# Kernel tuning notes

Measured on AMD Instinct MI355X. Metric: run time of the kernel, lower is better.

The kernel has to match this reference:

```python
import jax, jax.numpy as jnp
import numpy as np

B, N, E = 4, 25000, 1600000
NODE_DIM, EMBED = 64, 64
NUM = B * N


def setup_inputs() -> dict:
    key = jax.random.key(0)
    ks = jax.random.split(key, 12)
    p = lambda k, s: jax.random.normal(k, s, jnp.float32) * 0.05
    z = lambda s: jnp.zeros(s, jnp.float32)
    return {
        "node_feat": jax.random.normal(ks[0], (B, N, NODE_DIM), jnp.float32),
        "src": jax.random.randint(ks[1], (E,), 0, NUM),
        "dst": jax.random.randint(ks[2], (E,), 0, NUM),
        "edge_weight": jax.random.uniform(ks[3], (E,), jnp.float32),
        "h": z((NUM, EMBED)),
        "W_cz": p(ks[4], (NODE_DIM, EMBED)), "b_cz": z((EMBED,)),
        "W_cr": p(ks[5], (NODE_DIM, EMBED)), "b_cr": z((EMBED,)),
        "W_ch": p(ks[6], (NODE_DIM, EMBED)), "b_ch": z((EMBED,)),
        "W_lz": p(ks[7], (2 * EMBED, EMBED)), "b_lz": z((EMBED,)),
        "W_lr": p(ks[8], (2 * EMBED, EMBED)), "b_lr": z((EMBED,)),
        "W_lh": p(ks[9], (2 * EMBED, EMBED)), "b_lh": z((EMBED,)),
        "W_head": p(ks[10], (EMBED, 1)), "b_head": z((1,)),
    }


def gcn_conv(x, W, b, src, dst, ew):
    # PyG GCNConv: self-loops (fill=1) + symmetric normalization, then linear.
    n = x.shape[0]
    loop = jnp.arange(n)
    s = jnp.concatenate([src, loop])
    d = jnp.concatenate([dst, loop])
    w = jnp.concatenate([ew, jnp.ones((n,), x.dtype)])
    deg = jax.ops.segment_sum(w, d, num_segments=n)
    dinv = jnp.where(deg > 0, jax.lax.rsqrt(deg), 0.0)
    norm = dinv[s] * w * dinv[d]                      # [E+n]
    xw = x @ W                                        # [n, EMBED]
    out = jax.ops.segment_sum(xw[s] * norm[:, None], d, num_segments=n)
    return out + b


def tgcn_cell(x, h, src, dst, ew,
              W_cz, b_cz, W_cr, b_cr, W_ch, b_ch,
              W_lz, b_lz, W_lr, b_lr, W_lh, b_lh):
    Z = jax.nn.sigmoid(
        jnp.concatenate([gcn_conv(x, W_cz, b_cz, src, dst, ew), h], axis=1) @ W_lz + b_lz)
    R = jax.nn.sigmoid(
        jnp.concatenate([gcn_conv(x, W_cr, b_cr, src, dst, ew), h], axis=1) @ W_lr + b_lr)
    H_tilde = jnp.tanh(
        jnp.concatenate([gcn_conv(x, W_ch, b_ch, src, dst, ew), h * R], axis=1) @ W_lh + b_lh)
    return Z * h + (1.0 - Z) * H_tilde


def reference(node_feat, src, dst, edge_weight, h,
              W_cz, b_cz, W_cr, b_cr, W_ch, b_ch,
              W_lz, b_lz, W_lr, b_lr, W_lh, b_lh,
              W_head, b_head):
    Bv, Nv, _ = node_feat.shape
    x = node_feat.reshape(Bv * Nv, -1)
    h0 = tgcn_cell(x, h, src, dst, edge_weight,
                   W_cz, b_cz, W_cr, b_cr, W_ch, b_ch,
                   W_lz, b_lz, W_lr, b_lr, W_lh, b_lh)
    z = jax.nn.relu(h0)
    z = (z @ W_head + b_head).reshape(Bv, Nv, -1)
    return (z, h0)
```

## Files before the change

### kernel.cpp

```cpp
#include <hip/hip_runtime.h>
#include <hip/hip_fp16.h>
#include <stdint.h>

typedef unsigned long long u64;
typedef _Float16 half8 __attribute__((ext_vector_type(8)));
typedef float f32x4 __attribute__((ext_vector_type(4)));

#define EPB 6144
#define CAPC 5440

__device__ __forceinline__ float sigm(float x) { return 1.0f / (1.0f + __expf(-x)); }
__device__ __forceinline__ float tanhfast(float x) { return 1.0f - 2.0f / (__expf(2.0f * x) + 1.0f); }
__device__ __forceinline__ int rli(int v, int k) { return __builtin_amdgcn_readlane(v, k); }
__device__ __forceinline__ float rlf(float v, int k) {
    return __int_as_float(__builtin_amdgcn_readlane(__float_as_int(v), k));
}

__global__ void k_pre(const float* __restrict__ Wcz, const float* __restrict__ bcz,
                      const float* __restrict__ Wcr, const float* __restrict__ bcr,
                      const float* __restrict__ Wch, const float* __restrict__ bch,
                      const float* __restrict__ Wlz, const float* __restrict__ blz,
                      const float* __restrict__ Wlr, const float* __restrict__ blr,
                      const float* __restrict__ Wlh, const float* __restrict__ blh,
                      const float4* __restrict__ h4, __half* __restrict__ aggh,
                      __half* __restrict__ B1f, __half* __restrict__ B2f,
                      float* __restrict__ bias, int* __restrict__ cursor, int hq) {
    int bid = blockIdx.x;
    if (bid < 113) {
        int tid = bid * 256 + threadIdx.x;
        if (tid < 1024) cursor[tid] = 0;
        if (tid < 24576) {
            int k = tid / 192, nc = tid % 192;
            int g = nc >> 6, j = nc & 63;
            const float* Wc = (g == 0) ? Wcz : (g == 1) ? Wcr : Wch;
            const float* Wl = (g == 0) ? Wlz : (g == 1) ? Wlr : Wlh;
            float v;
            if (k < 64) {
                float acc = 0.f;
                for (int m = 0; m < 64; m++) acc += Wc[k * 64 + m] * Wl[m * 64 + j];
                v = acc;
            } else {
                v = (g < 2) ? Wl[k * 64 + j] : 0.f;
            }
            int kt = k >> 5, nt = nc >> 4;
            int lane = (((k >> 3) & 3) << 4) | (nc & 15);
            B1f[(((kt * 12 + nt) * 64 + lane) << 3) + (k & 7)] = (__half)v;
        } else if (tid < 24576 + 4096) {
            int t = tid - 24576;
            int k = t >> 6, nc = t & 63;
            float v = Wlh[(64 + k) * 64 + nc];
            int kt = k >> 5, nt = nc >> 4;
            int lane = (((k >> 3) & 3) << 4) | (nc & 15);
            B2f[(((kt * 4 + nt) * 64 + lane) << 3) + (k & 7)] = (__half)v;
        } else if (tid < 24576 + 4096 + 192) {
            int t = tid - 24576 - 4096;
            int g = t >> 6, j = t & 63;
            const float* bc = (g == 0) ? bcz : (g == 1) ? bcr : bch;
            const float* Wl = (g == 0) ? Wlz : (g == 1) ? Wlr : Wlh;
            const float* bl = (g == 0) ? blz : (g == 1) ? blr : blh;
            float acc = bl[j];
            for (int m = 0; m < 64; m++) acc += bc[m] * Wl[m * 64 + j];
            bias[t] = acc;
        }
    } else {
        int i = (bid - 113) * 256 + threadIdx.x;
        if (i < hq) {
            float4 hv = h4[i];
            int elem = i * 4;
            int node = elem >> 6, c = elem & 63;
            __half2* ho = (__half2*)(aggh + (((size_t)node) << 7) + 64 + c);
            ho[0] = __floats2half2_rn(hv.x, hv.y);
            ho[1] = __floats2half2_rn(hv.z, hv.w);
        }
    }
}

__global__ void __launch_bounds__(1024) k_bin(const int* __restrict__ src, const int* __restrict__ dst,
                                              const float* __restrict__ ew,
                                              int* __restrict__ cursor, u64* __restrict__ binned,
                                              int E, int R) {
    __shared__ u64 recs[EPB];
    __shared__ int hist[512];
    __shared__ int loff[512];
    __shared__ int curL[512];
    __shared__ int gbase[512];

    int tid = threadIdx.x;
    if (tid < 512) hist[tid] = 0;
    __syncthreads();

    int base = blockIdx.x * EPB;
    int cntE = min(EPB, E - base);

    u64 myrec[6];
    int myr[6];
#pragma unroll
    for (int j = 0; j < 6; j++) {
        int idx = tid + j * 1024;
        if (idx < cntE) {
            int e = base + idx;
            int d = dst[e], s = src[e];
            float w = ew[e];
            int r = d >> 8;
            myr[j] = r;
            myrec[j] = (u64)((unsigned)s | ((unsigned)(d & 255) << 17)) | ((u64)__float_as_uint(w) << 32);
            atomicAdd(&hist[r], 1);
        } else myr[j] = -1;
    }
    __syncthreads();

    if (tid < 64) {
        int sums[8], tot = 0;
#pragma unroll
        for (int q = 0; q < 8; q++) { sums[q] = hist[tid * 8 + q]; tot += sums[q]; }
        int scan = tot;
#pragma unroll
        for (int o = 1; o < 64; o <<= 1) {
            int v = __shfl_up(scan, o);
            if (tid >= o) scan += v;
        }
        int run = scan - tot;
#pragma unroll
        for (int q = 0; q < 8; q++) { loff[tid * 8 + q] = run; run += sums[q]; }
    }
    if (tid < 512) curL[tid] = 0;
    if (tid < R) {
        int hcnt = hist[tid];
        if (hcnt > 0) gbase[tid] = tid * CAPC + atomicAdd(&cursor[tid], hcnt);
    }
    __syncthreads();

#pragma unroll
    for (int j = 0; j < 6; j++) {
        if (myr[j] >= 0) {
            int p = atomicAdd(&curL[myr[j]], 1);
            recs[loff[myr[j]] + p] = myrec[j];
        }
    }
    __syncthreads();

    int wave = tid >> 6, lane = tid & 63;
    for (int r = wave; r < R; r += 16) {
        int len = hist[r];
        if (!len) continue;
        int gb = gbase[r], lo = loff[r];
        int capEnd = (r + 1) * CAPC;
        for (int i = lane; i < len; i += 64)
            if (gb + i < capEnd) binned[(size_t)(gb + i)] = recs[lo + i];
    }
}

__global__ void __launch_bounds__(1024) k_sort(const int* __restrict__ cursor,
                                               u64* __restrict__ binned,
                                               const float2* __restrict__ x2,
                                               float* __restrict__ dinv,
                                               __half2* __restrict__ xs2,
                                               int* __restrict__ off_g, int* __restrict__ len_g,
                                               int n) {
    __shared__ u64 srt[CAPC];
    __shared__ int hist[256];
    __shared__ int noff[256];
    __shared__ int cur[256];
    __shared__ u64 degw64[256];
    __shared__ float dvS[256];

    int r = blockIdx.x, tid = threadIdx.x;
    if (tid < 256) { hist[tid] = 0; degw64[tid] = 0ULL; }
    __syncthreads();

    int cnt = min(cursor[r], CAPC);
    u64* B = binned + (size_t)r * CAPC;

    for (int i = tid; i < cnt; i += 1024) {
        u64 m = B[i];
        int dl = ((unsigned)m >> 17) & 255;
        atomicAdd(&hist[dl], 1);
        float w = __uint_as_float((unsigned)(m >> 32));
        atomicAdd(&degw64[dl], (u64)(w * 4294967296.0f));
    }
    __syncthreads();

    if (tid < 64) {
        int s0 = hist[tid * 4], s1 = hist[tid * 4 + 1], s2 = hist[tid * 4 + 2], s3 = hist[tid * 4 + 3];
        int tot = s0 + s1 + s2 + s3;
        int scan = tot;
#pragma unroll
        for (int o = 1; o < 64; o <<= 1) {
            int v = __shfl_up(scan, o);
            if (tid >= o) scan += v;
        }
        int run = scan - tot;
        noff[tid * 4] = run; run += s0;
        noff[tid * 4 + 1] = run; run += s1;
        noff[tid * 4 + 2] = run; run += s2;
        noff[tid * 4 + 3] = run;
    }
    __syncthreads();

    if (tid < 256) {
        int node = r * 256 + tid;
        float deg = (float)degw64[tid] * 0x1p-32f;
        float dv = rsqrtf(1.0f + deg);
        if (node < n) {
            dinv[node] = dv;
            off_g[node] = r * CAPC + noff[tid];
            len_g[node] = hist[tid];
        }
        cur[tid] = noff[tid];
        dvS[tid] = dv;
    }
    __syncthreads();

    for (int i = tid; i < cnt; i += 1024) {
        u64 m = B[i];
        int dl = ((unsigned)m >> 17) & 255;
        int p = atomicAdd(&cur[dl], 1);
        srt[p] = (u64)((unsigned)m & 0x1FFFF) | (m & 0xFFFFFFFF00000000ULL);
    }
    __syncthreads();

    for (int i = tid; i < cnt; i += 1024) B[i] = srt[i];
    int nbase = r * 256;
    for (int i = tid; i < 256 * 32; i += 1024) {
        int nl = i >> 5, cp = i & 31;
        int node = nbase + nl;
        if (node < n) {
            float2 xv = x2[((size_t)node << 5) + cp];
            float dv = dvS[nl];
            xs2[((size_t)node << 5) + cp] = __floats2half2_rn(dv * xv.x, dv * xv.y);
        }
    }
}

__global__ void __launch_bounds__(256) k_gather(const int* __restrict__ off_g, const int* __restrict__ len_g,
                                                const u64* __restrict__ csr, const float* __restrict__ dinv,
                                                const __half* __restrict__ xs,
                                                __half* __restrict__ aggh, int n) {
    int lane = threadIdx.x & 63;
    int wid = __builtin_amdgcn_readfirstlane(threadIdx.x >> 6);
    int d = blockIdx.x * 4 + wid;
    if (d >= n) return;
    int o0 = off_g[d], L = len_g[d];
    float dd = dinv[d];
    float acc[16];
#pragma unroll
    for (int j = 0; j < 16; j++) acc[j] = 0.f;
    acc[0] = (float)xs[((size_t)d << 6) + lane];

    for (int base = 0; base < L; base += 64) {
        int c = min(64, L - base);
        u64 m = (lane < c) ? csr[(size_t)(o0 + base) + lane] : 0;
        int s_l = (unsigned)m & 0x1FFFF;
        float w_l = __uint_as_float((unsigned)(m >> 32));
        int k = 0;
        for (; k + 16 <= c; k += 16) {
            int ss[16]; float ww[16], xr[16];
#pragma unroll
            for (int j = 0; j < 16; j++) { ss[j] = rli(s_l, k + j); ww[j] = rlf(w_l, k + j); }
#pragma unroll
            for (int j = 0; j < 16; j++) xr[j] = (float)xs[((size_t)ss[j] << 6) + lane];
#pragma unroll
            for (int j = 0; j < 16; j++) acc[j] = fmaf(ww[j], xr[j], acc[j]);
        }
        for (; k + 4 <= c; k += 4) {
            int ss[4]; float ww[4], xr[4];
#pragma unroll
            for (int j = 0; j < 4; j++) { ss[j] = rli(s_l, k + j); ww[j] = rlf(w_l, k + j); }
#pragma unroll
            for (int j = 0; j < 4; j++) xr[j] = (float)xs[((size_t)ss[j] << 6) + lane];
#pragma unroll
            for (int j = 0; j < 4; j++) acc[j] = fmaf(ww[j], xr[j], acc[j]);
        }
        for (; k < c; k++) {
            int s0 = rli(s_l, k);
            float w0 = rlf(w_l, k);
            acc[0] = fmaf(w0, (float)xs[((size_t)s0 << 6) + lane], acc[0]);
        }
    }
    float s = ((acc[0] + acc[1]) + (acc[2] + acc[3])) + ((acc[4] + acc[5]) + (acc[6] + acc[7]))
            + ((acc[8] + acc[9]) + (acc[10] + acc[11])) + ((acc[12] + acc[13]) + (acc[14] + acc[15]));
    aggh[((size_t)d << 7) + lane] = (__half)(dd * s);
}

__global__ void __launch_bounds__(256, 2) k_node(
        const __half* __restrict__ aggh,
        const __half* __restrict__ B1f_g, const __half* __restrict__ B2f_g,
        const float* __restrict__ bias_g, const float* __restrict__ Whead,
        const float* __restrict__ bhead,
        float* __restrict__ out_head, float* __restrict__ out_h, int n) {

    __shared__ __half B1s[24576];
    __shared__ __half B2s[4096];
    __shared__ float biasS[192];
    __shared__ float whS[64];
    __shared__ __half hrb[4][16 * 72];

    int tid = threadIdx.x;
    {
        const uint4* s1 = (const uint4*)B1f_g; uint4* d1 = (uint4*)B1s;
        for (int i = tid; i < 3072; i += 256) d1[i] = s1[i];
        const uint4* s2 = (const uint4*)B2f_g; uint4* d2 = (uint4*)B2s;
        for (int i = tid; i < 512; i += 256) d2[i] = s2[i];
        if (tid < 192) biasS[tid] = bias_g[tid];
        if (tid < 64) whS[tid] = Whead[tid];
    }
    __syncthreads();

    int lane = tid & 63;
    int wave = tid >> 6;
    int quad = lane >> 4;
    int l15 = lane & 15;

    float bz4[4], br4[4], bh4[4], wh4[4];
#pragma unroll
    for (int nt = 0; nt < 4; nt++) {
        bz4[nt] = biasS[nt * 16 + l15];
        br4[nt] = biasS[64 + nt * 16 + l15];
        bh4[nt] = biasS[128 + nt * 16 + l15];
        wh4[nt] = whS[nt * 16 + l15];
    }
    float bhv = bhead[0];
    __half* myhr = &hrb[wave][0];
    const half8* B1v = (const half8*)B1s;
    const half8* B2v = (const half8*)B2s;

    int mbase = blockIdx.x * 64 + wave * 16;
    if (mbase < n) {
        const half8* arow = (const half8*)(aggh + (((size_t)(mbase + l15)) << 7) + (quad << 3));
        half8 a0 = arow[0], a1 = arow[4], a2 = arow[8], a3 = arow[12];

        f32x4 acc[12];
#pragma unroll
        for (int nt = 0; nt < 12; nt++) acc[nt] = (f32x4){0.f, 0.f, 0.f, 0.f};

#pragma unroll
        for (int nt = 0; nt < 12; nt++) {
            acc[nt] = __builtin_amdgcn_mfma_f32_16x16x32_f16(a0, B1v[(0 * 12 + nt) * 64 + lane], acc[nt], 0, 0, 0);
            acc[nt] = __builtin_amdgcn_mfma_f32_16x16x32_f16(a1, B1v[(1 * 12 + nt) * 64 + lane], acc[nt], 0, 0, 0);
            acc[nt] = __builtin_amdgcn_mfma_f32_16x16x32_f16(a2, B1v[(2 * 12 + nt) * 64 + lane], acc[nt], 0, 0, 0);
            acc[nt] = __builtin_amdgcn_mfma_f32_16x16x32_f16(a3, B1v[(3 * 12 + nt) * 64 + lane], acc[nt], 0, 0, 0);
        }

        float hv[4][4];
#pragma unroll
        for (int nt = 0; nt < 4; nt++)
#pragma unroll
            for (int r = 0; r < 4; r++)
                hv[nt][r] = (float)aggh[(((size_t)(mbase + quad * 4 + r)) << 7) + 64 + nt * 16 + l15];

        float Z[4][4];
#pragma unroll
        for (int nt = 0; nt < 4; nt++)
#pragma unroll
            for (int r = 0; r < 4; r++) {
                Z[nt][r] = sigm(acc[nt][r] + bz4[nt]);
                float R = sigm(acc[4 + nt][r] + br4[nt]);
                myhr[(quad * 4 + r) * 72 + nt * 16 + l15] = (__half)(hv[nt][r] * R);
            }
        __builtin_amdgcn_s_waitcnt(0);

        half8 a2f0 = *(const half8*)(myhr + l15 * 72 + quad * 8);
        half8 a2f1 = *(const half8*)(myhr + l15 * 72 + 32 + quad * 8);

#pragma unroll
        for (int nt = 0; nt < 4; nt++) {
            acc[8 + nt] = __builtin_amdgcn_mfma_f32_16x16x32_f16(a2f0, B2v[(0 * 4 + nt) * 64 + lane], acc[8 + nt], 0, 0, 0);
            acc[8 + nt] = __builtin_amdgcn_mfma_f32_16x16x32_f16(a2f1, B2v[(1 * 4 + nt) * 64 + lane], acc[8 + nt], 0, 0, 0);
        }

        float pr0 = 0.f, pr1 = 0.f, pr2 = 0.f, pr3 = 0.f;
#pragma unroll
        for (int nt = 0; nt < 4; nt++) {
#pragma unroll
            for (int r = 0; r < 4; r++) {
                float Ht = tanhfast(acc[8 + nt][r] + bh4[nt]);
                float z = Z[nt][r];
                float hn = z * hv[nt][r] + (1.f - z) * Ht;
                out_h[((size_t)(mbase + quad * 4 + r)) * 64 + nt * 16 + l15] = hn;
                float rv = fmaxf(hn, 0.f) * wh4[nt];
                if (r == 0) pr0 += rv; else if (r == 1) pr1 += rv; else if (r == 2) pr2 += rv; else pr3 += rv;
            }
        }
#pragma unroll
        for (int o = 1; o < 16; o <<= 1) {
            pr0 += __shfl_xor(pr0, o);
            pr1 += __shfl_xor(pr1, o);
            pr2 += __shfl_xor(pr2, o);
            pr3 += __shfl_xor(pr3, o);
        }
        if (l15 == 0) {
            out_head[mbase + quad * 4 + 0] = pr0 + bhv;
            out_head[mbase + quad * 4 + 1] = pr1 + bhv;
            out_head[mbase + quad * 4 + 2] = pr2 + bhv;
            out_head[mbase + quad * 4 + 3] = pr3 + bhv;
        }
    }
}

extern "C" void kernel_launch(void* const* d_in, const int* in_sizes, int n_in,
                              void* d_out, int out_size, void* d_ws, size_t ws_size,
                              hipStream_t stream) {
    const float* x     = (const float*)d_in[0];
    const int*   src   = (const int*)d_in[1];
    const int*   dst   = (const int*)d_in[2];
    const float* ew    = (const float*)d_in[3];
    const float* h     = (const float*)d_in[4];
    const float* Wcz   = (const float*)d_in[5];
    const float* bcz   = (const float*)d_in[6];
    const float* Wcr   = (const float*)d_in[7];
    const float* bcr   = (const float*)d_in[8];
    const float* Wch   = (const float*)d_in[9];
    const float* bch   = (const float*)d_in[10];
    const float* Wlz   = (const float*)d_in[11];
    const float* blz   = (const float*)d_in[12];
    const float* Wlr   = (const float*)d_in[13];
    const float* blr   = (const float*)d_in[14];
    const float* Wlh   = (const float*)d_in[15];
    const float* blh   = (const float*)d_in[16];
    const float* Whead = (const float*)d_in[17];
    const float* bhead = (const float*)d_in[18];

    int E = in_sizes[1];
    int n = in_sizes[4] / 64;
    int R = (n + 255) >> 8;

    __half* aggh = (__half*)d_ws;
    __half* xs   = aggh + (size_t)n * 128;
    u64*   binned = (u64*)(xs + (size_t)n * 64);
    float* dinv  = (float*)(binned + (size_t)R * CAPC);
    int*   off_g = (int*)(dinv + n);
    int*   len_g = off_g + n;
    int*   cursor = len_g + n;
    __half* B1f  = (__half*)(cursor + 1024);
    __half* B2f  = B1f + 24576;
    float* bias  = (float*)(B2f + 4096);

    float* out_head = (float*)d_out;
    float* out_h    = out_head + n;

    int hq = n * 16;
    int nbB = (E + EPB - 1) / EPB;
    int gridPre = 113 + (hq + 255) / 256;

    k_pre<<<gridPre, 256, 0, stream>>>(Wcz, bcz, Wcr, bcr, Wch, bch,
                                       Wlz, blz, Wlr, blr, Wlh, blh,
                                       (const float4*)h, aggh, B1f, B2f, bias, cursor, hq);
    k_bin<<<nbB, 1024, 0, stream>>>(src, dst, ew, cursor, binned, E, R);
    k_sort<<<R, 1024, 0, stream>>>(cursor, binned, (const float2*)x, dinv,
                                   (__half2*)xs, off_g, len_g, n);
    k_gather<<<(n + 3) / 4, 256, 0, stream>>>(off_g, len_g, binned, dinv, xs, aggh, n);
    k_node<<<(n + 63) / 64, 256, 0, stream>>>(aggh, B1f, B2f, bias, Whead, bhead,
                                              out_head, out_h, n);
}
```

Measured before the change: 235.2 us.

## Build CSR with global atomic counting, block scan and atomic scatter

Replaces the two-level LDS binning and per-bin sort with a direct CSR build. A per-edge global 64-bit atomic packs the in-degree count and the fixed-point weighted degree for each destination node. A block-level scan then turns counts into offsets, taking each block's base from an atomic cursor, and a final pass scatters each edge into its slot with a per-node atomic cursor. This removes the staging buffer with fixed per-bin capacity and its extra read/write passes, but adds many contended global atomics and random 8-byte writes. Edge order within a node, and the placement of node ranges, become nondeterministic.

Result: slower. 413.9 us (+76.0%).

```diff
diff --git a/kernel.cpp b/kernel.cpp
--- a/kernel.cpp
+++ b/kernel.cpp
@@ -5,9 +5,6 @@
 typedef unsigned long long u64;
 typedef _Float16 half8 __attribute__((ext_vector_type(8)));
 typedef float f32x4 __attribute__((ext_vector_type(4)));
-
-#define EPB 6144
-#define CAPC 5440
 
 __device__ __forceinline__ float sigm(float x) { return 1.0f / (1.0f + __expf(-x)); }
 __device__ __forceinline__ float tanhfast(float x) { return 1.0f - 2.0f / (__expf(2.0f * x) + 1.0f); }
@@ -16,19 +13,26 @@
     return __int_as_float(__builtin_amdgcn_readlane(__float_as_int(v), k));
 }
 
-__global__ void k_pre(const float* __restrict__ Wcz, const float* __restrict__ bcz,
-                      const float* __restrict__ Wcr, const float* __restrict__ bcr,
-                      const float* __restrict__ Wch, const float* __restrict__ bch,
-                      const float* __restrict__ Wlz, const float* __restrict__ blz,
-                      const float* __restrict__ Wlr, const float* __restrict__ blr,
-                      const float* __restrict__ Wlh, const float* __restrict__ blh,
-                      const float4* __restrict__ h4, __half* __restrict__ aggh,
-                      __half* __restrict__ B1f, __half* __restrict__ B2f,
-                      float* __restrict__ bias, int* __restrict__ cursor, int hq) {
+__global__ void k_zero(u64* __restrict__ cntdeg, int* __restrict__ gcur, int n) {
+    int i = blockIdx.x * 256 + threadIdx.x;
+    if (i < n) cntdeg[i] = 0ULL;
+    if (i < 16) gcur[i] = 0;
+}
+
+__global__ void k_prec(const float* __restrict__ Wcz, const float* __restrict__ bcz,
+                       const float* __restrict__ Wcr, const float* __restrict__ bcr,
+                       const float* __restrict__ Wch, const float* __restrict__ bch,
+                       const float* __restrict__ Wlz, const float* __restrict__ blz,
+                       const float* __restrict__ Wlr, const float* __restrict__ blr,
+                       const float* __restrict__ Wlh, const float* __restrict__ blh,
+                       const float4* __restrict__ h4, __half* __restrict__ aggh,
+                       __half* __restrict__ B1f, __half* __restrict__ B2f,
+                       float* __restrict__ bias,
+                       const int* __restrict__ dst, const float* __restrict__ ew,
+                       u64* __restrict__ cntdeg, int hq, int E, int hb) {
     int bid = blockIdx.x;
     if (bid < 113) {
         int tid = bid * 256 + threadIdx.x;
-        if (tid < 1024) cursor[tid] = 0;
         if (tid < 24576) {
             int k = tid / 192, nc = tid % 192;
             int g = nc >> 6, j = nc & 63;
@@ -62,7 +66,7 @@
             for (int m = 0; m < 64; m++) acc += bc[m] * Wl[m * 64 + j];
             bias[t] = acc;
         }
-    } else {
+    } else if (bid < 113 + hb) {
         int i = (bid - 113) * 256 + threadIdx.x;
         if (i < hq) {
             float4 hv = h4[i];
@@ -72,164 +76,88 @@
             ho[0] = __floats2half2_rn(hv.x, hv.y);
             ho[1] = __floats2half2_rn(hv.z, hv.w);
         }
-    }
-}
-
-__global__ void __launch_bounds__(1024) k_bin(const int* __restrict__ src, const int* __restrict__ dst,
-                                              const float* __restrict__ ew,
-                                              int* __restrict__ cursor, u64* __restrict__ binned,
-                                              int E, int R) {
-    __shared__ u64 recs[EPB];
-    __shared__ int hist[512];
-    __shared__ int loff[512];
-    __shared__ int curL[512];
-    __shared__ int gbase[512];
+    } else {
+        int e = (bid - 113 - hb) * 256 + threadIdx.x;
+        if (e < E) {
+            int d = dst[e];
+            float w = ew[e];
+            atomicAdd(&cntdeg[d], (1ULL << 48) | (u64)(w * 4294967296.0f));
+        }
+    }
+}
+
+__global__ void __launch_bounds__(1024) k_scan(const u64* __restrict__ cntdeg,
+                                               const float2* __restrict__ x2,
+                                               int* __restrict__ off_g, int* __restrict__ len_g,
+                                               int* __restrict__ cur_g, float* __restrict__ dinv,
+                                               __half2* __restrict__ xs2,
+                                               int* __restrict__ gcur, int n) {
+    __shared__ int wsum[16];
+    __shared__ int sbase;
+    __shared__ float dvS[1024];
 
     int tid = threadIdx.x;
-    if (tid < 512) hist[tid] = 0;
+    int nb = blockIdx.x * 1024;
+    int node = nb + tid;
+    u64 v = (node < n) ? cntdeg[node] : 0ULL;
+    int c = (int)(v >> 48);
+    float deg = (float)(v & 0xFFFFFFFFFFFFULL) * 0x1p-32f;
+
+    int lane = tid & 63, wv = tid >> 6;
+    int scan = c;
+#pragma unroll
+    for (int o = 1; o < 64; o <<= 1) {
+        int t = __shfl_up(scan, o);
+        if (lane >= o) scan += t;
+    }
+    if (lane == 63) wsum[wv] = scan;
     __syncthreads();
-
-    int base = blockIdx.x * EPB;
-    int cntE = min(EPB, E - base);
-
-    u64 myrec[6];
-    int myr[6];
-#pragma unroll
-    for (int j = 0; j < 6; j++) {
-        int idx = tid + j * 1024;
-        if (idx < cntE) {
-            int e = base + idx;
-            int d = dst[e], s = src[e];
-            float w = ew[e];
-            int r = d >> 8;
-            myr[j] = r;
-            myrec[j] = (u64)((unsigned)s | ((unsigned)(d & 255) << 17)) | ((u64)__float_as_uint(w) << 32);
-            atomicAdd(&hist[r], 1);
-        } else myr[j] = -1;
+    if (tid < 16) {
+        int s = wsum[tid];
+        int sc = s;
+#pragma unroll
+        for (int o = 1; o < 16; o <<= 1) {
+            int t = __shfl_up(sc, o);
+            if (tid >= o) sc += t;
+        }
+        wsum[tid] = sc - s;
+        if (tid == 15) sbase = atomicAdd(gcur, sc);
     }
     __syncthreads();
 
-    if (tid < 64) {
-        int sums[8], tot = 0;
-#pragma unroll
-        for (int q = 0; q < 8; q++) { sums[q] = hist[tid * 8 + q]; tot += sums[q]; }
-        int scan = tot;
-#pragma unroll
-        for (int o = 1; o < 64; o <<= 1) {
-            int v = __shfl_up(scan, o);
-            if (tid >= o) scan += v;
-        }
-        int run = scan - tot;
-#pragma unroll
-        for (int q = 0; q < 8; q++) { loff[tid * 8 + q] = run; run += sums[q]; }
-    }
-    if (tid < 512) curL[tid] = 0;
-    if (tid < R) {
-        int hcnt = hist[tid];
-        if (hcnt > 0) gbase[tid] = tid * CAPC + atomicAdd(&cursor[tid], hcnt);
-    }
+    int excl = (scan - c) + wsum[wv] + sbase;
+    float dv = rsqrtf(1.0f + deg);
+    if (node < n) {
+        off_g[node] = excl;
+        cur_g[node] = excl;
+        len_g[node] = c;
+        dinv[node]  = dv;
+    }
+    dvS[tid] = dv;
     __syncthreads();
 
-#pragma unroll
-    for (int j = 0; j < 6; j++) {
-        if (myr[j] >= 0) {
-            int p = atomicAdd(&curL[myr[j]], 1);
-            recs[loff[myr[j]] + p] = myrec[j];
-        }
-    }
-    __syncthreads();
-
-    int wave = tid >> 6, lane = tid & 63;
-    for (int r = wave; r < R; r += 16) {
-        int len = hist[r];
-        if (!len) continue;
-        int gb = gbase[r], lo = loff[r];
-        int capEnd = (r + 1) * CAPC;
-        for (int i = lane; i < len; i += 64)
-            if (gb + i < capEnd) binned[(size_t)(gb + i)] = recs[lo + i];
-    }
-}
-
-__global__ void __launch_bounds__(1024) k_sort(const int* __restrict__ cursor,
-                                               u64* __restrict__ binned,
-                                               const float2* __restrict__ x2,
-                                               float* __restrict__ dinv,
-                                               __half2* __restrict__ xs2,
-                                               int* __restrict__ off_g, int* __restrict__ len_g,
-                                               int n) {
-    __shared__ u64 srt[CAPC];
-    __shared__ int hist[256];
-    __shared__ int noff[256];
-    __shared__ int cur[256];
-    __shared__ u64 degw64[256];
-    __shared__ float dvS[256];
-
-    int r = blockIdx.x, tid = threadIdx.x;
-    if (tid < 256) { hist[tid] = 0; degw64[tid] = 0ULL; }
-    __syncthreads();
-
-    int cnt = min(cursor[r], CAPC);
-    u64* B = binned + (size_t)r * CAPC;
-
-    for (int i = tid; i < cnt; i += 1024) {
-        u64 m = B[i];
-        int dl = ((unsigned)m >> 17) & 255;
-        atomicAdd(&hist[dl], 1);
-        float w = __uint_as_float((unsigned)(m >> 32));
-        atomicAdd(&degw64[dl], (u64)(w * 4294967296.0f));
-    }
-    __syncthreads();
-
-    if (tid < 64) {
-        int s0 = hist[tid * 4], s1 = hist[tid * 4 + 1], s2 = hist[tid * 4 + 2], s3 = hist[tid * 4 + 3];
-        int tot = s0 + s1 + s2 + s3;
-        int scan = tot;
-#pragma unroll
-        for (int o = 1; o < 64; o <<= 1) {
-            int v = __shfl_up(scan, o);
-            if (tid >= o) scan += v;
-        }
-        int run = scan - tot;
-        noff[tid * 4] = run; run += s0;
-        noff[tid * 4 + 1] = run; run += s1;
-        noff[tid * 4 + 2] = run; run += s2;
-        noff[tid * 4 + 3] = run;
-    }
-    __syncthreads();
-
-    if (tid < 256) {
-        int node = r * 256 + tid;
-        float deg = (float)degw64[tid] * 0x1p-32f;
-        float dv = rsqrtf(1.0f + deg);
-        if (node < n) {
-            dinv[node] = dv;
-            off_g[node] = r * CAPC + noff[tid];
-            len_g[node] = hist[tid];
-        }
-        cur[tid] = noff[tid];
-        dvS[tid] = dv;
-    }
-    __syncthreads();
-
-    for (int i = tid; i < cnt; i += 1024) {
-        u64 m = B[i];
-        int dl = ((unsigned)m >> 17) & 255;
-        int p = atomicAdd(&cur[dl], 1);
-        srt[p] = (u64)((unsigned)m & 0x1FFFF) | (m & 0xFFFFFFFF00000000ULL);
-    }
-    __syncthreads();
-
-    for (int i = tid; i < cnt; i += 1024) B[i] = srt[i];
-    int nbase = r * 256;
-    for (int i = tid; i < 256 * 32; i += 1024) {
+    for (int i = tid; i < 1024 * 32; i += 1024) {
         int nl = i >> 5, cp = i & 31;
-        int node = nbase + nl;
-        if (node < n) {
-            float2 xv = x2[((size_t)node << 5) + cp];
-            float dv = dvS[nl];
-            xs2[((size_t)node << 5) + cp] = __floats2half2_rn(dv * xv.x, dv * xv.y);
-        }
-    }
+        int nd = nb + nl;
+        if (nd < n) {
+            float2 xv = x2[((size_t)nd << 5) + cp];
+            float d2 = dvS[nl];
+            xs2[((size_t)nd << 5) + cp] = __floats2half2_rn(d2 * xv.x, d2 * xv.y);
+        }
+    }
+}
+
+__global__ void __launch_bounds__(1024) k_scatter(const int* __restrict__ src,
+                                                  const int* __restrict__ dst,
+                                                  const float* __restrict__ ew,
+                                                  int* __restrict__ cur_g,
+                                                  u64* __restrict__ csr, int E) {
+    int e = blockIdx.x * 1024 + threadIdx.x;
+    if (e >= E) return;
+    int s = src[e], d = dst[e];
+    float w = ew[e];
+    int slot = atomicAdd(&cur_g[d], 1);
+    csr[slot] = (u64)(unsigned)s | ((u64)__float_as_uint(w) << 32);
 }
 
 __global__ void __launch_bounds__(256) k_gather(const int* __restrict__ off_g, const int* __restrict__ len_g,
@@ -422,16 +350,17 @@
 
     int E = in_sizes[1];
     int n = in_sizes[4] / 64;
-    int R = (n + 255) >> 8;
 
     __half* aggh = (__half*)d_ws;
     __half* xs   = aggh + (size_t)n * 128;
-    u64*   binned = (u64*)(xs + (size_t)n * 64);
-    float* dinv  = (float*)(binned + (size_t)R * CAPC);
-    int*   off_g = (int*)(dinv + n);
+    u64*   csr   = (u64*)(xs + (size_t)n * 64);
+    u64*   cntdeg = csr + (size_t)E;
+    int*   gcur  = (int*)(cntdeg + n);
+    int*   off_g = gcur + 16;
     int*   len_g = off_g + n;
-    int*   cursor = len_g + n;
-    __half* B1f  = (__half*)(cursor + 1024);
+    int*   cur_g = len_g + n;
+    float* dinv  = (float*)(cur_g + n);
+    __half* B1f  = (__half*)(dinv + n);
     __half* B2f  = B1f + 24576;
     float* bias  = (float*)(B2f + 4096);
 
@@ -439,16 +368,19 @@
     float* out_h    = out_head + n;
 
     int hq = n * 16;
-    int nbB = (E + EPB - 1) / EPB;
-    int gridPre = 113 + (hq + 255) / 256;
-
-    k_pre<<<gridPre, 256, 0, stream>>>(Wcz, bcz, Wcr, bcr, Wch, bch,
-                                       Wlz, blz, Wlr, blr, Wlh, blh,
-                                       (const float4*)h, aggh, B1f, B2f, bias, cursor, hq);
-    k_bin<<<nbB, 1024, 0, stream>>>(src, dst, ew, cursor, binned, E, R);
-    k_sort<<<R, 1024, 0, stream>>>(cursor, binned, (const float2*)x, dinv,
-                                   (__half2*)xs, off_g, len_g, n);
-    k_gather<<<(n + 3) / 4, 256, 0, stream>>>(off_g, len_g, binned, dinv, xs, aggh, n);
+    int hb = (hq + 255) / 256;
+    int eb = (E + 255) / 256;
+
+    k_zero<<<(n + 255) / 256, 256, 0, stream>>>(cntdeg, gcur, n);
+    k_prec<<<113 + hb + eb, 256, 0, stream>>>(Wcz, bcz, Wcr, bcr, Wch, bch,
+                                              Wlz, blz, Wlr, blr, Wlh, blh,
+                                              (const float4*)h, aggh, B1f, B2f, bias,
+                                              dst, ew, cntdeg, hq, E, hb);
+    k_scan<<<(n + 1023) / 1024, 1024, 0, stream>>>(cntdeg, (const float2*)x,
+                                                   off_g, len_g, cur_g, dinv,
+                                                   (__half2*)xs, gcur, n);
+    k_scatter<<<(E + 1023) / 1024, 1024, 0, stream>>>(src, dst, ew, cur_g, csr, E);
+    k_gather<<<(n + 3) / 4, 256, 0, stream>>>(off_g, len_g, csr, dinv, xs, aggh, n);
     k_node<<<(n + 63) / 64, 256, 0, stream>>>(aggh, B1f, B2f, bias, Whead, bhead,
                                               out_head, out_h, n);
 }
```
